# Kernel tuning notes

Hardware: AMD Instinct MI355X
Metric: run time of the kernel (lower is better)

The kernel has to match this reference:

```python
import jax, jax.numpy as jnp
import numpy as np

N_FFT = 256
HOP = 64
K = 2       # top-k experts
E = 8       # num experts


def conv1d(x, w, b, stride, pad):
    # x: [B, Cin, L], w: [Cout, Cin, Kw]
    y = jax.lax.conv_general_dilated(x, w, (stride,), [(pad, pad)],
                                     dimension_numbers=('NCH', 'OIH', 'NCH'))
    return y + b[None, :, None]


def stft_mag(x):
    # torch.stft(center=True, pad_mode='reflect', hann window, onesided)
    pad = N_FFT // 2
    xp = jnp.pad(x, ((0, 0), (pad, pad)), mode='reflect')
    n_frames = 1 + (xp.shape[1] - N_FFT) // HOP
    idx = jnp.arange(n_frames)[:, None] * HOP + jnp.arange(N_FFT)[None, :]
    win = 0.5 - 0.5 * jnp.cos(2.0 * jnp.pi * jnp.arange(N_FFT) / N_FFT)  # periodic hann
    frames = xp[:, idx] * win            # [B, F, n_fft]
    return jnp.abs(jnp.fft.rfft(frames, axis=-1))  # [B, F, n_fft//2+1]


def expert_fwd(x, wa3, ba3, wb3, bb3, wa5, ba5, wb5, bb5, wa7, ba7, wb7, bb7):
    # MultiScalePyramidBranch: 3 parallel conv branches (k=3/5/7), 2 conv layers each
    xc = x[:, None, :]  # [B, 1, L]
    outs = []
    for wa, ba, wb, bb in ((wa3, ba3, wb3, bb3), (wa5, ba5, wb5, bb5), (wa7, ba7, wb7, bb7)):
        h = jax.nn.relu(conv1d(xc, wa, ba, 2, wa.shape[-1] // 2))
        h = jax.nn.relu(conv1d(h, wb, bb, 2, 1))
        outs.append(h)
    return jnp.concatenate(outs, axis=1)  # [B, 192, L//4]


def moe_forward(x, Wg1, bg1, Wg2, bg2, Wg3, bg3, ew):
    # gating on frequency domain (stft is computed under no_grad in the original)
    mag = stft_mag(jax.lax.stop_gradient(x))
    pooled = mag.mean(axis=1)                     # adaptive_avg_pool1d(.,1) over frames
    h = jax.nn.relu(pooled @ Wg1 + bg1)
    h = jax.nn.relu(h @ Wg2 + bg2)
    logits = h @ Wg3 + bg3                        # [B, E]
    vals, inds = jax.lax.top_k(logits, K)
    w = jax.nn.softmax(vals, axis=1)              # softmax over the top-k weights
    # vectorized dispatch: run all experts on the whole batch, then gather+combine
    all_out = jax.vmap(expert_fwd, in_axes=(None,) + (0,) * 12)(x, *ew)  # [E, B, C, T]
    B = x.shape[0]
    bidx = jnp.arange(B)
    out = jnp.zeros_like(all_out[0])
    for j in range(K):
        out = out + w[:, j, None, None] * all_out[inds[:, j], bidx]
    return out


def setup_inputs() -> dict:
    key = jax.random.key(0)
    ks = jax.random.split(key, 20)

    def p(k, shape, s=0.02):
        return (s * jax.random.normal(k, shape)).astype(jnp.float32)

    inp = {'x': jax.random.normal(ks[0], (64, 4096), dtype=jnp.float32)}
    inp['Wg1'] = p(ks[1], (129, 256)); inp['bg1'] = jnp.zeros((256,), jnp.float32)
    inp['Wg2'] = p(ks[2], (256, 128)); inp['bg2'] = jnp.zeros((128,), jnp.float32)
    inp['Wg3'] = p(ks[3], (128, E));   inp['bg3'] = jnp.zeros((E,), jnp.float32)
    i = 4
    for ksz in (3, 5, 7):
        inp['wa%d' % ksz] = p(ks[i], (E, 64, 1, ksz)); i += 1
        inp['ba%d' % ksz] = jnp.zeros((E, 64), jnp.float32)
        inp['wb%d' % ksz] = p(ks[i], (E, 64, 64, 3)); i += 1
        inp['bb%d' % ksz] = jnp.zeros((E, 64), jnp.float32)
    return inp


def reference(x, Wg1, bg1, Wg2, bg2, Wg3, bg3,
              wa3, ba3, wb3, bb3, wa5, ba5, wb5, bb5, wa7, ba7, wb7, bb7):
    ew = (wa3, ba3, wb3, bb3, wa5, ba5, wb5, bb5, wa7, ba7, wb7, bb7)
    return moe_forward(x, Wg1, bg1, Wg2, bg2, Wg3, bg3, ew)
```

## Files before the change

kernel.cpp:

```cpp
#include <hip/hip_runtime.h>
#include <math.h>

#define NFFT 256
#define NBINS 129
#define HOP 64
#define NFRAMES 65
#define NB 64
#define LX 4096
#define LH 2048
#define LY 1024
#define NCH 64
#define NBR 3
#define NE 8

#define NFG 13
#define PART_STRIDE 132
#define PART_ZERO 440320
#define WTF_OFF 440320
#define WTF_PER 98304
#define IW_OFF 1031168

typedef __attribute__((ext_vector_type(8))) short short8;
typedef __attribute__((ext_vector_type(4))) float floatx4;

__device__ __forceinline__ unsigned short bf16r(float f) {
    unsigned u = __builtin_bit_cast(unsigned, f);
    u += 0x7FFFu + ((u >> 16) & 1u);
    return (unsigned short)(u >> 16);
}

__global__ __launch_bounds__(128) void stft_kernel(
    const float* __restrict__ x,
    const float* __restrict__ wb3, const float* __restrict__ wb5,
    const float* __restrict__ wb7, unsigned short* __restrict__ wTf,
    float* __restrict__ part) {
    __shared__ float xw[NFFT];
    const int f = blockIdx.x, b = blockIdx.y;
    const int tid = threadIdx.x;

    {
        int bid = b * NFRAMES + f;
        for (int fi = bid * 128 + tid; fi < 3 * WTF_PER;
             fi += NB * NFRAMES * 128) {
            int br = fi / WTF_PER, r = fi % WTF_PER;
            int e = r / 12288;
            int r2 = r % 12288;
            int mw = r2 / 3072;
            int r3 = r2 % 3072;
            int i = r3 / 1024;
            int r4 = r3 % 1024;
            int kb = r4 / 512;
            int r5 = r4 % 512;
            int lane = r5 / 8, j = r5 % 8;
            int c2 = mw * 16 + (lane & 15);
            int cl = kb * 32 + (lane >> 4) * 8 + j;
            const float* src = (br == 0) ? wb3 : (br == 1) ? wb5 : wb7;
            wTf[fi] = bf16r(src[((e * 64 + c2) * 64 + cl) * 3 + i]);
        }
    }

    for (int n = tid; n < NFFT; n += 128) {
        float a2 = (float)(2.0 * 3.14159265358979323846 / 256.0) * (float)n;
        float sn, cn;
        sincosf(a2, &sn, &cn);
        float win = 0.5f - 0.5f * cn;
        int q = f * HOP + n - 128;
        int xi = q < 0 ? -q : (q >= LX ? (2 * LX - 2 - q) : q);
        xw[n] = x[b * LX + xi] * win;
    }
    __syncthreads();

    const int k = tid;
    float ang = (float)(2.0 * 3.14159265358979323846 / 256.0) * (float)k;
    float s1, c1;
    sincosf(ang, &s1, &c1);

    float A0 = 0.f, B0 = 0.f, A1 = 0.f, B1 = 0.f;
    float A2 = 0.f, B2 = 0.f, A3 = 0.f, B3 = 0.f;
    float c0 = 1.f, s0 = 0.f, cc1 = 1.f, ss1 = 0.f;
    float cc2 = 1.f, ss2 = 0.f, cc3 = 1.f, ss3 = 0.f;
    float rNe = 0.f, rNo = 0.f;

#pragma unroll 4
    for (int mq = 0; mq < 16; ++mq) {
        float4 v0 = *(const float4*)&xw[4 * mq];
        float4 v1 = *(const float4*)&xw[64 + 4 * mq];
        float4 v2 = *(const float4*)&xw[128 + 4 * mq];
        float4 v3 = *(const float4*)&xw[192 + 4 * mq];
        float e0[4] = {v0.x, v0.y, v0.z, v0.w};
        float e1[4] = {v1.x, v1.y, v1.z, v1.w};
        float e2[4] = {v2.x, v2.y, v2.z, v2.w};
        float e3[4] = {v3.x, v3.y, v3.z, v3.w};
#pragma unroll
        for (int mm = 0; mm < 4; ++mm) {
            float t;
            A0 = fmaf(e0[mm], c0, A0);  B0 = fmaf(e0[mm], s0, B0);
            A1 = fmaf(e1[mm], cc1, A1); B1 = fmaf(e1[mm], ss1, B1);
            A2 = fmaf(e2[mm], cc2, A2); B2 = fmaf(e2[mm], ss2, B2);
            A3 = fmaf(e3[mm], cc3, A3); B3 = fmaf(e3[mm], ss3, B3);
            if ((mm & 1) == 0) rNe += e0[mm] + e1[mm] + e2[mm] + e3[mm];
            else               rNo += e0[mm] + e1[mm] + e2[mm] + e3[mm];
            t = c0 * c1 - s0 * s1;   s0 = fmaf(c0, s1, s0 * c1);   c0 = t;
            t = cc1 * c1 - ss1 * s1; ss1 = fmaf(cc1, s1, ss1 * c1); cc1 = t;
            t = cc2 * c1 - ss2 * s1; ss2 = fmaf(cc2, s1, ss2 * c1); cc2 = t;
            t = cc3 * c1 - ss3 * s1; ss3 = fmaf(cc3, s1, ss3 * c1); cc3 = t;
        }
    }

    float re = A0, im = B0;
    float Aj[3] = {A1, A2, A3};
    float Bj[3] = {B1, B2, B3};
#pragma unroll
    for (int j = 1; j < 4; ++j) {
        int ph = (j * k) & 3;
        float cf = (ph == 0) ? 1.f : (ph == 2) ? -1.f : 0.f;
        float sf = (ph == 1) ? 1.f : (ph == 3) ? -1.f : 0.f;
        re += cf * Aj[j - 1] - sf * Bj[j - 1];
        im += sf * Aj[j - 1] + cf * Bj[j - 1];
    }

    float* prow = part + (b * NFG + f / 5) * PART_STRIDE;
    atomicAdd(&prow[k], sqrtf(re * re + im * im));
    if (tid == 0) atomicAdd(&prow[128], fabsf(rNe - rNo));
}

__global__ __launch_bounds__(256) void gating_kernel(
    const float* __restrict__ part,
    const float* __restrict__ Wg1, const float* __restrict__ bg1,
    const float* __restrict__ Wg2, const float* __restrict__ bg2,
    const float* __restrict__ Wg3, const float* __restrict__ bg3,
    int* __restrict__ inds, float* __restrict__ wts) {
    __shared__ float pl[NBINS];
    __shared__ float h1[256];
    __shared__ float h2[128];
    __shared__ float lg[NE];
    const int b = blockIdx.x, tid = threadIdx.x;

    if (tid < NBINS) {
        float s = 0.f;
        for (int g = 0; g < NFG; ++g)
            s += part[(b * NFG + g) * PART_STRIDE + tid];
        pl[tid] = s * (1.0f / (float)NFRAMES);
    }
    __syncthreads();
    {
        float s = bg1[tid];
        for (int kk = 0; kk < NBINS; ++kk) s += pl[kk] * Wg1[kk * 256 + tid];
        h1[tid] = fmaxf(s, 0.f);
    }
    __syncthreads();
    if (tid < 128) {
        float s = bg2[tid];
        for (int kk = 0; kk < 256; ++kk) s += h1[kk] * Wg2[kk * 128 + tid];
        h2[tid] = fmaxf(s, 0.f);
    }
    __syncthreads();
    if (tid < NE) {
        float s = bg3[tid];
        for (int kk = 0; kk < 128; ++kk) s += h2[kk] * Wg3[kk * NE + tid];
        lg[tid] = s;
    }
    __syncthreads();
    if (tid == 0) {
        int i0 = 0;
        float v0 = lg[0];
        for (int i = 1; i < NE; ++i)
            if (lg[i] > v0) { v0 = lg[i]; i0 = i; }
        int i1 = -1;
        float v1 = -3.0e38f;
        for (int i = 0; i < NE; ++i) {
            if (i == i0) continue;
            if (lg[i] > v1) { v1 = lg[i]; i1 = i; }
        }
        float e1 = expf(v1 - v0);
        float w0 = 1.f / (1.f + e1);
        inds[b * 2 + 0] = i0;
        inds[b * 2 + 1] = i1;
        wts[b * 2 + 0] = w0;
        wts[b * 2 + 1] = e1 * w0;
    }
}

#define UT 128
#define HPR 68
#define HROWS 258

template <int KSZ>
__device__ __attribute__((always_inline)) void expert_body(
    const float* __restrict__ x,
    const float* __restrict__ wa, const float* __restrict__ ba,
    const float* __restrict__ bb, const unsigned short* __restrict__ wTfbr,
    const int* __restrict__ inds, const float* __restrict__ wts,
    float* __restrict__ out, int br, short* hp) {
    const int u0 = blockIdx.x * UT;
    const int b = blockIdx.z;
    const int tid = threadIdx.x;
    const int lane = tid & 63;
    const int quad = lane >> 4;
    const int l15 = lane & 15;
    const int wv = __builtin_amdgcn_readfirstlane(tid >> 6);
    const int mw = wv & 3;
    const int nh = wv >> 2;
    const int pad = KSZ >> 1;
    const int t0 = 2 * u0 - 1;
    const int x0 = 2 * t0 - pad;

    const float* xp = x + b * LX;

    float fin[4][4];
#pragma unroll
    for (int q = 0; q < 4; ++q)
#pragma unroll
        for (int r = 0; r < 4; ++r) fin[q][r] = 0.f;

#pragma unroll 1
    for (int slot = 0; slot < 2; ++slot) {
        const int e = __builtin_amdgcn_readfirstlane(inds[b * 2 + slot]);
        const float wj = wts[b * 2 + slot];

        float wr[KSZ];
#pragma unroll
        for (int i = 0; i < KSZ; ++i) wr[i] = wa[(e * NCH + lane) * KSZ + i];
        const float bv = ba[e * NCH + lane];

        __syncthreads();

#pragma unroll 1
        for (int it = 0; it < 9; ++it) {
            int tb = wv + 8 * it;
            if (tb > 64) break;
            int base = x0 + 8 * tb;
            float xr[16];
            if (base >= 0 && base + 15 < LX) {
#pragma unroll
                for (int ii = 0; ii < 16; ++ii) xr[ii] = xp[base + ii];
            } else {
#pragma unroll
                for (int ii = 0; ii < 16; ++ii) {
                    int xi = base + ii;
                    xr[ii] = (xi >= 0 && xi < LX) ? xp[xi] : 0.f;
                }
            }
#pragma unroll
            for (int m = 0; m < 4; ++m) {
                int tl = 4 * tb + m;
                if (tl > 257) continue;
                int t = t0 + tl;
                float s = bv;
#pragma unroll
                for (int i = 0; i < KSZ; ++i) s += wr[i] * xr[2 * m + i];
                float h = (t >= 0 && t < LH) ? fmaxf(s, 0.f) : 0.f;
                hp[tl * HPR + lane] = (short)bf16r(h);
            }
        }
        __syncthreads();

        float br4[4];
#pragma unroll
        for (int r = 0; r < 4; ++r)
            br4[r] = bb[e * NCH + mw * 16 + quad * 4 + r];

        short8 af[3][2];
        {
            const unsigned short* wbase =
                wTfbr + e * 12288 + mw * 3072 + lane * 8;
#pragma unroll
            for (int i = 0; i < 3; ++i)
#pragma unroll
                for (int kb = 0; kb < 2; ++kb)
                    af[i][kb] = *(const short8*)&wbase[i * 1024 + kb * 512];
        }

#pragma unroll 1
        for (int q = 0; q < 4; ++q) {
            int nt = nh * 4 + q;
            int nb = nt * 16 + l15;
            floatx4 acc = {br4[0], br4[1], br4[2], br4[3]};
#pragma unroll
            for (int i = 0; i < 3; ++i) {
                int tl = 2 * nb + i;
#pragma unroll
                for (int kb = 0; kb < 2; ++kb) {
                    int sb = tl * HPR + kb * 32 + quad * 8;
                    union { short8 v; unsigned long long q2[2]; } B;
                    B.q2[0] = *(const unsigned long long*)&hp[sb];
                    B.q2[1] = *(const unsigned long long*)&hp[sb + 4];
                    acc = __builtin_amdgcn_mfma_f32_16x16x32_bf16(
                        af[i][kb], B.v, acc, 0, 0, 0);
                }
            }
#pragma unroll
            for (int r = 0; r < 4; ++r)
                fin[q][r] += wj * fmaxf(acc[r], 0.f);
        }
    }

#pragma unroll
    for (int q = 0; q < 4; ++q) {
        int u = u0 + (nh * 4 + q) * 16 + l15;
#pragma unroll
        for (int r = 0; r < 4; ++r) {
            int c2 = mw * 16 + quad * 4 + r;
            out[(long)(b * 192 + br * 64 + c2) * LY + u] = fin[q][r];
        }
    }
}

__global__ __launch_bounds__(512, 2) void expert_kernel(
    const float* __restrict__ x,
    const float* __restrict__ wa3, const float* __restrict__ ba3,
    const float* __restrict__ bb3,
    const float* __restrict__ wa5, const float* __restrict__ ba5,
    const float* __restrict__ bb5,
    const float* __restrict__ wa7, const float* __restrict__ ba7,
    const float* __restrict__ bb7,
    const unsigned short* __restrict__ wTf,
    const int* __restrict__ inds, const float* __restrict__ wts,
    float* __restrict__ out) {
    __shared__ short hp[HROWS * HPR];

    const int br = blockIdx.y;
    if (br == 0)
        expert_body<3>(x, wa3, ba3, bb3, wTf, inds, wts, out, 0, hp);
    else if (br == 1)
        expert_body<5>(x, wa5, ba5, bb5, wTf + WTF_PER, inds, wts, out, 1, hp);
    else
        expert_body<7>(x, wa7, ba7, bb7, wTf + 2 * WTF_PER, inds, wts, out, 2, hp);
}

extern "C" void kernel_launch(void* const* d_in, const int* in_sizes, int n_in,
                              void* d_out, int out_size, void* d_ws, size_t ws_size,
                              hipStream_t stream) {
    const float* x   = (const float*)d_in[0];
    const float* Wg1 = (const float*)d_in[1];
    const float* bg1 = (const float*)d_in[2];
    const float* Wg2 = (const float*)d_in[3];
    const float* bg2 = (const float*)d_in[4];
    const float* Wg3 = (const float*)d_in[5];
    const float* bg3 = (const float*)d_in[6];
    const float* wa3 = (const float*)d_in[7];
    const float* ba3 = (const float*)d_in[8];
    const float* wb3 = (const float*)d_in[9];
    const float* bb3 = (const float*)d_in[10];
    const float* wa5 = (const float*)d_in[11];
    const float* ba5 = (const float*)d_in[12];
    const float* wb5 = (const float*)d_in[13];
    const float* bb5 = (const float*)d_in[14];
    const float* wa7 = (const float*)d_in[15];
    const float* ba7 = (const float*)d_in[16];
    const float* wb7 = (const float*)d_in[17];
    const float* bb7 = (const float*)d_in[18];

    float* part = (float*)d_ws;
    unsigned short* wTf = (unsigned short*)((char*)d_ws + WTF_OFF);
    int* inds = (int*)((char*)d_ws + IW_OFF);
    float* wts = (float*)((char*)d_ws + IW_OFF + 512);

    hipMemsetAsync(d_ws, 0, PART_ZERO, stream);
    stft_kernel<<<dim3(NFRAMES, NB), 128, 0, stream>>>(x, wb3, wb5, wb7, wTf,
                                                       part);
    gating_kernel<<<NB, 256, 0, stream>>>(part, Wg1, bg1, Wg2, bg2, Wg3, bg3,
                                          inds, wts);
    expert_kernel<<<dim3(LY / UT, NBR, NB), 512, 0, stream>>>(
        x, wa3, ba3, bb3, wa5, ba5, bb5, wa7, ba7, bb7, wTf,
        inds, wts, (float*)d_out);
}
```

Measured before the change: 179.8 us.

## Drop atomics and memset in STFT, move weight repack to gating kernel

The STFT kernel now writes per-frame magnitudes directly instead of atomically accumulating into frame groups, which removes the memset launch and atomic contention. The gating kernel sums all 65 frames itself and also takes over the bf16 weight repacking from the STFT kernel. The expert phase-A loop is split into a helper with fixed trip counts and partial unrolling, and the MFMA loop is unrolled by 2. In exchange the partial buffer is larger, and the repack now runs on only 64 blocks, which can lengthen the serial gating stage.

```diff
diff --git a/kernel.cpp b/kernel.cpp
--- a/kernel.cpp
+++ b/kernel.cpp
@@ -13,12 +13,11 @@
 #define NBR 3
 #define NE 8
 
-#define NFG 13
 #define PART_STRIDE 132
-#define PART_ZERO 440320
-#define WTF_OFF 440320
+#define PART_BYTES (NB * NFRAMES * PART_STRIDE * 4)
+#define WTF_OFF 2197504
 #define WTF_PER 98304
-#define IW_OFF 1031168
+#define IW_OFF 2787328
 
 typedef __attribute__((ext_vector_type(8))) short short8;
 typedef __attribute__((ext_vector_type(4))) float floatx4;
@@ -30,34 +29,10 @@
 }
 
 __global__ __launch_bounds__(128) void stft_kernel(
-    const float* __restrict__ x,
-    const float* __restrict__ wb3, const float* __restrict__ wb5,
-    const float* __restrict__ wb7, unsigned short* __restrict__ wTf,
-    float* __restrict__ part) {
+    const float* __restrict__ x, float* __restrict__ part) {
     __shared__ float xw[NFFT];
     const int f = blockIdx.x, b = blockIdx.y;
     const int tid = threadIdx.x;
-
-    {
-        int bid = b * NFRAMES + f;
-        for (int fi = bid * 128 + tid; fi < 3 * WTF_PER;
-             fi += NB * NFRAMES * 128) {
-            int br = fi / WTF_PER, r = fi % WTF_PER;
-            int e = r / 12288;
-            int r2 = r % 12288;
-            int mw = r2 / 3072;
-            int r3 = r2 % 3072;
-            int i = r3 / 1024;
-            int r4 = r3 % 1024;
-            int kb = r4 / 512;
-            int r5 = r4 % 512;
-            int lane = r5 / 8, j = r5 % 8;
-            int c2 = mw * 16 + (lane & 15);
-            int cl = kb * 32 + (lane >> 4) * 8 + j;
-            const float* src = (br == 0) ? wb3 : (br == 1) ? wb5 : wb7;
-            wTf[fi] = bf16r(src[((e * 64 + c2) * 64 + cl) * 3 + i]);
-        }
-    }
 
     for (int n = tid; n < NFFT; n += 128) {
         float a2 = (float)(2.0 * 3.14159265358979323846 / 256.0) * (float)n;
@@ -119,9 +94,9 @@
         im += sf * Aj[j - 1] + cf * Bj[j - 1];
     }
 
-    float* prow = part + (b * NFG + f / 5) * PART_STRIDE;
-    atomicAdd(&prow[k], sqrtf(re * re + im * im));
-    if (tid == 0) atomicAdd(&prow[128], fabsf(rNe - rNo));
+    float* prow = part + (b * NFRAMES + f) * PART_STRIDE;
+    prow[k] = sqrtf(re * re + im * im);
+    if (tid == 0) prow[128] = fabsf(rNe - rNo);
 }
 
 __global__ __launch_bounds__(256) void gating_kernel(
@@ -129,6 +104,8 @@
     const float* __restrict__ Wg1, const float* __restrict__ bg1,
     const float* __restrict__ Wg2, const float* __restrict__ bg2,
     const float* __restrict__ Wg3, const float* __restrict__ bg3,
+    const float* __restrict__ wb3, const float* __restrict__ wb5,
+    const float* __restrict__ wb7, unsigned short* __restrict__ wTf,
     int* __restrict__ inds, float* __restrict__ wts) {
     __shared__ float pl[NBINS];
     __shared__ float h1[256];
@@ -136,10 +113,27 @@
     __shared__ float lg[NE];
     const int b = blockIdx.x, tid = threadIdx.x;
 
+    for (int fi = b * 256 + tid; fi < 3 * WTF_PER; fi += NB * 256) {
+        int br = fi / WTF_PER, r = fi % WTF_PER;
+        int e = r / 12288;
+        int r2 = r % 12288;
+        int mw = r2 / 3072;
+        int r3 = r2 % 3072;
+        int i = r3 / 1024;
+        int r4 = r3 % 1024;
+        int kb = r4 / 512;
+        int r5 = r4 % 512;
+        int lane = r5 / 8, j = r5 % 8;
+        int c2 = mw * 16 + (lane & 15);
+        int cl = kb * 32 + (lane >> 4) * 8 + j;
+        const float* src = (br == 0) ? wb3 : (br == 1) ? wb5 : wb7;
+        wTf[fi] = bf16r(src[((e * 64 + c2) * 64 + cl) * 3 + i]);
+    }
+
     if (tid < NBINS) {
         float s = 0.f;
-        for (int g = 0; g < NFG; ++g)
-            s += part[(b * NFG + g) * PART_STRIDE + tid];
+        for (int f = 0; f < NFRAMES; ++f)
+            s += part[(b * NFRAMES + f) * PART_STRIDE + tid];
         pl[tid] = s * (1.0f / (float)NFRAMES);
     }
     __syncthreads();
@@ -184,6 +178,36 @@
 #define UT 128
 #define HPR 68
 #define HROWS 258
+
+template <int KSZ>
+__device__ __forceinline__ void phaseA_rows(
+    const float* __restrict__ xp, const float* wr, float bv, short* hp,
+    int tb, int nrow, int t0, int x0) {
+    const int lane_cl = threadIdx.x & 63;
+    int base = x0 + 8 * tb;
+    float xr[16];
+    if (base >= 0 && base + 15 < LX) {
+#pragma unroll
+        for (int ii = 0; ii < 16; ++ii) xr[ii] = xp[base + ii];
+    } else {
+#pragma unroll
+        for (int ii = 0; ii < 16; ++ii) {
+            int xi = base + ii;
+            xr[ii] = (xi >= 0 && xi < LX) ? xp[xi] : 0.f;
+        }
+    }
+#pragma unroll
+    for (int m = 0; m < 4; ++m) {
+        if (m >= nrow) break;
+        int tl = 4 * tb + m;
+        int t = t0 + tl;
+        float s = bv;
+#pragma unroll
+        for (int i = 0; i < KSZ; ++i) s += wr[i] * xr[2 * m + i];
+        float h = (t >= 0 && t < LH) ? fmaxf(s, 0.f) : 0.f;
+        hp[tl * HPR + lane_cl] = (short)bf16r(h);
+    }
+}
 
 template <int KSZ>
 __device__ __attribute__((always_inline)) void expert_body(
@@ -225,34 +249,11 @@
 
         __syncthreads();
 
-#pragma unroll 1
-        for (int it = 0; it < 9; ++it) {
-            int tb = wv + 8 * it;
-            if (tb > 64) break;
-            int base = x0 + 8 * tb;
-            float xr[16];
-            if (base >= 0 && base + 15 < LX) {
-#pragma unroll
-                for (int ii = 0; ii < 16; ++ii) xr[ii] = xp[base + ii];
-            } else {
-#pragma unroll
-                for (int ii = 0; ii < 16; ++ii) {
-                    int xi = base + ii;
-                    xr[ii] = (xi >= 0 && xi < LX) ? xp[xi] : 0.f;
-                }
-            }
-#pragma unroll
-            for (int m = 0; m < 4; ++m) {
-                int tl = 4 * tb + m;
-                if (tl > 257) continue;
-                int t = t0 + tl;
-                float s = bv;
-#pragma unroll
-                for (int i = 0; i < KSZ; ++i) s += wr[i] * xr[2 * m + i];
-                float h = (t >= 0 && t < LH) ? fmaxf(s, 0.f) : 0.f;
-                hp[tl * HPR + lane] = (short)bf16r(h);
-            }
-        }
+#pragma unroll 2
+        for (int it = 0; it < 8; ++it)
+            phaseA_rows<KSZ>(xp, wr, bv, hp, wv + 8 * it, 4, t0, x0);
+        if (wv == 0)
+            phaseA_rows<KSZ>(xp, wr, bv, hp, 64, 2, t0, x0);
         __syncthreads();
 
         float br4[4];
@@ -271,7 +272,7 @@
                     af[i][kb] = *(const short8*)&wbase[i * 1024 + kb * 512];
         }
 
-#pragma unroll 1
+#pragma unroll 2
         for (int q = 0; q < 4; ++q) {
             int nt = nh * 4 + q;
             int nb = nt * 16 + l15;
@@ -356,11 +357,9 @@
     int* inds = (int*)((char*)d_ws + IW_OFF);
     float* wts = (float*)((char*)d_ws + IW_OFF + 512);
 
-    hipMemsetAsync(d_ws, 0, PART_ZERO, stream);
-    stft_kernel<<<dim3(NFRAMES, NB), 128, 0, stream>>>(x, wb3, wb5, wb7, wTf,
-                                                       part);
+    stft_kernel<<<dim3(NFRAMES, NB), 128, 0, stream>>>(x, part);
     gating_kernel<<<NB, 256, 0, stream>>>(part, Wg1, bg1, Wg2, bg2, Wg3, bg3,
-                                          inds, wts);
+                                          wb3, wb5, wb7, wTf, inds, wts);
     expert_kernel<<<dim3(LY / UT, NBR, NB), 512, 0, stream>>>(
         x, wa3, ba3, bb3, wa5, ba5, bb5, wa7, ba7, bb7, wTf,
         inds, wts, (float*)d_out);
```

New measurement: 185.0 us. +2.9%, slower.
